# Kernel tuning notes

Measured on AMD Instinct MI355X. Metric: run time of the kernel, lower is better.

## Reference

```python
import jax, jax.numpy as jnp
import numpy as np

N_NODES = 8192
N_EDGES = 262144
HIDDEN = 256
EDGE_DIM = 64


def _lin(x, w, b=None):
    y = x @ w.T
    return y if b is None else y + b


def _gru(m, h, wih, whh, bih, bhh):
    # torch.nn.GRUCell math
    gi = m @ wih.T + bih
    gh = h @ whh.T + bhh
    i_r, i_z, i_n = jnp.split(gi, 3, axis=-1)
    h_r, h_z, h_n = jnp.split(gh, 3, axis=-1)
    r = jax.nn.sigmoid(i_r + h_r)
    z = jax.nn.sigmoid(i_z + h_z)
    n = jnp.tanh(i_n + r * h_n)
    return (1.0 - z) * n + z * h


def _dmpnn(x, src, dst, edge_attr, w_msg, wih, whh, bih, bhh):
    # message: W_msg([x_j ; e]) gathered at src, scatter-add to dst, GRU update
    msg = jnp.concatenate([x[src], edge_attr], axis=-1) @ w_msg.T  # [E,H]
    m = jax.ops.segment_sum(msg, dst, num_segments=x.shape[0])     # [N,H]
    return _gru(m, x, wih, whh, bih, bhh)


def _gin(x, src, dst, w1, b1, w2, b2):
    # GINConv with eps=0: mlp(x + sum_j x_j)
    agg = jax.ops.segment_sum(x[src], dst, num_segments=x.shape[0])
    return _lin(jax.nn.relu(_lin(x + agg, w1, b1)), w2, b2)


def setup_inputs():
    key = jax.random.key(0)
    ks = iter(jax.random.split(key, 48))
    def nrm(shape, scale=0.05):
        return jax.random.normal(next(ks), shape, dtype=jnp.float32) * scale
    H, ED = HIDDEN, EDGE_DIM
    inp = {}
    inp['x'] = nrm((N_NODES, H), 1.0)
    inp['edge_index'] = jax.random.randint(next(ks), (2, N_EDGES), 0, N_NODES, dtype=jnp.int32)
    inp['edge_attr'] = nrm((N_EDGES, ED), 1.0)
    inp['rc_mask'] = jax.random.randint(next(ks), (N_NODES,), 0, 20) == 0
    for i in (1, 2):
        inp[f'W_msg{i}'] = nrm((H, H + ED))
        inp[f'gru{i}_wih'] = nrm((3 * H, H))
        inp[f'gru{i}_whh'] = nrm((3 * H, H))
        inp[f'gru{i}_bih'] = jnp.zeros((3 * H,), jnp.float32)
        inp[f'gru{i}_bhh'] = jnp.zeros((3 * H,), jnp.float32)
    inp['gin_w1'] = nrm((3, H, H)); inp['gin_b1'] = jnp.zeros((3, H), jnp.float32)
    inp['gin_w2'] = nrm((3, H, H)); inp['gin_b2'] = jnp.zeros((3, H), jnp.float32)
    inp['proj_w'] = nrm((H, 3 * H)); inp['proj_b'] = jnp.zeros((H,), jnp.float32)
    for nm in ('q', 'k', 'v', 'o'):
        inp[f'{nm}_w'] = nrm((H, H)); inp[f'{nm}_b'] = jnp.zeros((H,), jnp.float32)
    inp['gate_w1'] = nrm((H // 2, H)); inp['gate_b1'] = jnp.zeros((H // 2,), jnp.float32)
    inp['gate_w2'] = nrm((1, H // 2)); inp['gate_b2'] = jnp.zeros((1,), jnp.float32)
    inp['skip_W'] = nrm((H, H))
    inp['sgru_wih'] = nrm((3 * H, H)); inp['sgru_whh'] = nrm((3 * H, H))
    inp['sgru_bih'] = jnp.zeros((3 * H,), jnp.float32); inp['sgru_bhh'] = jnp.zeros((3 * H,), jnp.float32)
    inp['rc_init'] = nrm((1, H)); inp['s_init'] = nrm((1, H))
    return inp


def reference(x, edge_index, edge_attr, rc_mask,
              W_msg1, gru1_wih, gru1_whh, gru1_bih, gru1_bhh,
              W_msg2, gru2_wih, gru2_whh, gru2_bih, gru2_bhh,
              gin_w1, gin_b1, gin_w2, gin_b2, proj_w, proj_b,
              q_w, q_b, k_w, k_b, v_w, v_b, o_w, o_b,
              gate_w1, gate_b1, gate_w2, gate_b2, skip_W,
              sgru_wih, sgru_whh, sgru_bih, sgru_bhh, rc_init, s_init):
    src, dst = edge_index[0], edge_index[1]
    N = x.shape[0]
    H = x.shape[1]
    # AtomDMPNN: two DMPNN layers
    h = _dmpnn(x, src, dst, edge_attr, W_msg1, gru1_wih, gru1_whh, gru1_bih, gru1_bhh)
    h = _dmpnn(h, src, dst, edge_attr, W_msg2, gru2_wih, gru2_whh, gru2_bih, gru2_bhh)
    # MixHop: 1-,2-,3-hop GINs, concat, project
    outs = []
    for i, hop in enumerate((1, 2, 3)):
        t = h
        for _ in range(hop):
            t = _gin(t, src, dst, gin_w1[i], gin_b1[i], gin_w2[i], gin_b2[i])
        outs.append(t)
    h_mix = _lin(jnp.concatenate(outs, axis=-1), proj_w, proj_b)  # [N,H]
    # add RC supernode (idx N) and S supernode (idx N+1)
    hh = jnp.concatenate([h_mix, rc_init, s_init], axis=0)  # [N+2,H]
    # GatedSkipBlock: masked non-RC atoms -> S
    atoms = hh[:N]
    alpha = jax.nn.sigmoid(_lin(jax.nn.relu(_lin(atoms, gate_w1, gate_b1)), gate_w2, gate_b2))  # [N,1]
    msgs = alpha * (atoms @ skip_W.T)
    non_rc = (~rc_mask).astype(hh.dtype)[:, None]
    m_sum = jnp.sum(msgs * non_rc, axis=0, keepdims=True)
    m_rc = hh[N:N + 1] @ skip_W.T  # h[-2:-1] is the RC node
    h_S = _gru(m_sum + m_rc, hh[N + 1:N + 2], sgru_wih, sgru_whh, sgru_bih, sgru_bhh)
    hh = hh.at[N + 1].set(h_S[0])
    # dense self-attention over all N+2 nodes
    q = _lin(hh, q_w, q_b)
    k = _lin(hh, k_w, k_b)
    v = _lin(hh, v_w, v_b)
    attn = jax.nn.softmax((q @ k.T) / jnp.sqrt(jnp.asarray(H, hh.dtype)), axis=-1)
    h_attn = hh + _lin(attn @ v, o_w, o_b)
    # jumping-knowledge max with zero-padded mixhop features
    h_pad = jnp.pad(h_mix, ((0, 2), (0, 0)))
    h_jk = jnp.maximum(h_pad, h_attn)
    return h_jk[N + 1]
```

## Files before the change

### kernel.cpp

```cpp
#include <hip/hip_runtime.h>
#include <hip/hip_bf16.h>

#define NN   8192
#define NE   262144
#define HD   256
#define NHH  8194

using f32x4  = __attribute__((ext_vector_type(4))) float;
using bf16x8 = __attribute__((ext_vector_type(8))) short;
typedef unsigned short u16;

#define GAS(p) ((const __attribute__((address_space(1))) void*)(p))
#define LAS(p) ((__attribute__((address_space(3))) void*)(p))

__device__ __forceinline__ u16 f2bf(float f) {
    unsigned u = __builtin_bit_cast(unsigned, f);
    u = (u + 0x7FFFu + ((u >> 16) & 1u)) >> 16;
    return (u16)u;
}
__device__ __forceinline__ float bf2f(u16 h) {
    return __builtin_bit_cast(float, (unsigned)h << 16);
}
__device__ __forceinline__ void split1(float a, u16& h, u16& l) {
    h = f2bf(a);
    l = f2bf(a - bf2f(h));
}
__device__ __forceinline__ void store_split4(u16* hi, u16* lo, size_t off, float4 v) {
    ushort4 h, l;
    split1(v.x, h.x, l.x); split1(v.y, h.y, l.y);
    split1(v.z, h.z, l.z); split1(v.w, h.w, l.w);
    *(ushort4*)(hi + off) = h;
    *(ushort4*)(lo + off) = l;
}
__device__ __forceinline__ void add4(float4& a, float4 b) {
    a.x += b.x; a.y += b.y; a.z += b.z; a.w += b.w;
}

__global__ void hist_kernel(const int* __restrict__ dst, int* __restrict__ cnt, int E) {
    int e = blockIdx.x * blockDim.x + threadIdx.x;
    if (e < E) atomicAdd(&cnt[dst[e]], 1);
}

__global__ __launch_bounds__(1024) void scan_kernel(const int* __restrict__ cnt, int* __restrict__ row_ptr) {
    __shared__ int sdata[1024];
    int tid = threadIdx.x;
    int v[8], local[8];
    int s = 0;
#pragma unroll
    for (int i = 0; i < 8; i++) v[i] = cnt[tid * 8 + i];
#pragma unroll
    for (int i = 0; i < 8; i++) { local[i] = s; s += v[i]; }
    sdata[tid] = s;
    __syncthreads();
    for (int off = 1; off < 1024; off <<= 1) {
        int t = (tid >= off) ? sdata[tid - off] : 0;
        __syncthreads();
        sdata[tid] += t;
        __syncthreads();
    }
    int base = (tid == 0) ? 0 : sdata[tid - 1];
#pragma unroll
    for (int i = 0; i < 8; i++) row_ptr[tid * 8 + i] = base + local[i];
    if (tid == 1023) row_ptr[8192] = sdata[1023];
}

__global__ void copy_int_kernel(const int* __restrict__ a, int* __restrict__ b, int n) {
    int i = blockIdx.x * blockDim.x + threadIdx.x;
    if (i < n) b[i] = a[i];
}

__global__ void fill_kernel(const int* __restrict__ dst, const int* __restrict__ src,
                            int* __restrict__ cursor, int* __restrict__ eids,
                            int* __restrict__ gsrc, int E) {
    int e = blockIdx.x * blockDim.x + threadIdx.x;
    if (e < E) {
        int pos = atomicAdd(&cursor[dst[e]], 1);
        eids[pos] = e;
        gsrc[pos] = src[e];
    }
}

struct SplitArgs {
    const float* src[11];
    u16* hi[11];
    u16* lo[11];
    int  off[12];
};
__global__ __launch_bounds__(256) void multisplit_kernel(SplitArgs a) {
    int blk = blockIdx.x;
    int s = 0;
#pragma unroll
    for (int t = 0; t < 11; ++t) if (blk >= a.off[t + 1]) s = t + 1;
    size_t i = ((size_t)(blk - a.off[s]) * 256 + threadIdx.x) * 4;
    float4 v = *(const float4*)(a.src[s] + i);
    store_split4(a.hi[s], a.lo[s], i, v);
}

__global__ void wtrans_split_kernel(const float* __restrict__ W, u16* __restrict__ outh,
                                    u16* __restrict__ outl, int R, int Cc) {
    int j = blockIdx.x * 256 + threadIdx.x;
    if (j >= R * Cc) return;
    int r = j % R, c = j / R;
    u16 h, l;
    split1(W[(size_t)r * Cc + c], h, l);
    outh[j] = h; outl[j] = l;
}

struct SegDuo {
    const float* T0; u16* oh0; u16* ol0; int self0;
    const float* T1; u16* oh1; u16* ol1; int self1; int nb0;
};
__global__ __launch_bounds__(256) void segsum128_wave_kernel(const int* __restrict__ row_ptr,
                                                             const int* __restrict__ idx,
                                                             SegDuo a) {
    int blk  = blockIdx.x;
    int seg  = blk / a.nb0;
    int lblk = blk - seg * a.nb0;
    const float* T; u16* oh; u16* ol; int self;
    if (seg >> 1) { T = a.T1; oh = a.oh1; ol = a.ol1; self = a.self1; }
    else          { T = a.T0; oh = a.oh0; ol = a.ol0; self = a.self0; }
    const int half = seg & 1;
    const int n    = lblk * 4 + (threadIdx.x >> 6);
    const int lane = threadIdx.x & 63;
    const int slot = lane >> 5;
    const size_t fo = (size_t)half * 128 + (size_t)(lane & 31) * 4;
    const int b = row_ptr[n], e = row_ptr[n + 1];
    float4 z4 = make_float4(0.f, 0.f, 0.f, 0.f);
    float4 a0 = z4, a1 = z4, a2 = z4, a3 = z4;
    int i = b + slot;
    for (; i + 6 < e; i += 8) {
        int s0 = idx[i], s1 = idx[i + 2], s2 = idx[i + 4], s3 = idx[i + 6];
        add4(a0, *(const float4*)(T + (size_t)s0 * HD + fo));
        add4(a1, *(const float4*)(T + (size_t)s1 * HD + fo));
        add4(a2, *(const float4*)(T + (size_t)s2 * HD + fo));
        add4(a3, *(const float4*)(T + (size_t)s3 * HD + fo));
    }
    for (; i < e; i += 2) {
        int s0 = idx[i];
        add4(a0, *(const float4*)(T + (size_t)s0 * HD + fo));
    }
    if (self && slot == 0) add4(a1, *(const float4*)(T + (size_t)n * HD + fo));
    add4(a0, a1); add4(a2, a3); add4(a0, a2);
    a0.x += __shfl_xor(a0.x, 32); a0.y += __shfl_xor(a0.y, 32);
    a0.z += __shfl_xor(a0.z, 32); a0.w += __shfl_xor(a0.w, 32);
    if (slot == 0) store_split4(oh, ol, (size_t)n * HD + fo, a0);
}

__global__ __launch_bounds__(256) void segsum64_wave_kernel(const int* __restrict__ row_ptr,
                                                            const int* __restrict__ idx,
                                                            const float* __restrict__ T,
                                                            u16* __restrict__ outh,
                                                            u16* __restrict__ outl) {
    const int n    = blockIdx.x * 4 + (threadIdx.x >> 6);
    const int lane = threadIdx.x & 63;
    const int g    = lane >> 4;
    const size_t fo = (size_t)(lane & 15) * 4;
    const int b = row_ptr[n], e = row_ptr[n + 1];
    float4 a0 = make_float4(0.f, 0.f, 0.f, 0.f);
    float4 a1 = a0;
    int i = b + g;
    for (; i + 4 < e; i += 8) {
        int s0 = idx[i], s1 = idx[i + 4];
        add4(a0, *(const float4*)(T + (size_t)s0 * 64 + fo));
        add4(a1, *(const float4*)(T + (size_t)s1 * 64 + fo));
    }
    if (i < e) {
        int s0 = idx[i];
        add4(a0, *(const float4*)(T + (size_t)s0 * 64 + fo));
    }
    add4(a0, a1);
    a0.x += __shfl_xor(a0.x, 16); a0.y += __shfl_xor(a0.y, 16);
    a0.z += __shfl_xor(a0.z, 16); a0.w += __shfl_xor(a0.w, 16);
    a0.x += __shfl_xor(a0.x, 32); a0.y += __shfl_xor(a0.y, 32);
    a0.z += __shfl_xor(a0.z, 32); a0.w += __shfl_xor(a0.w, 32);
    if (g == 0) store_split4(outh, outl, (size_t)n * 64 + fo, a0);
}

struct GDesc {
    const u16 *Ah, *Al, *Abh, *Abl, *Wh, *Wl;
    const float* bias;
    float* C; u16 *Chi, *Clo;
    int lda, ldab, Ka, Kb, ldw, ldc, M, flags, nbx, nblk;
};
struct GBatch { GDesc d[3]; int start[4]; };

#define LDSA0 0
#define LDSA1 8192
#define LDSW0 16384
#define LDSW1 20480
__global__ __launch_bounds__(256) void hgemm_kernel(GBatch b) {
    __shared__ __align__(16) u16 lds[24576];
    int s = (blockIdx.x >= (unsigned)b.start[1]) + (blockIdx.x >= (unsigned)b.start[2]);
    GDesc d = b.d[0];
    if (s == 1) d = b.d[1];
    else if (s == 2) d = b.d[2];

    int nwg = b.start[s + 1] - b.start[s];
    int o   = blockIdx.x - b.start[s];
    int q = nwg >> 3, r = nwg & 7;
    int xcd = o & 7;
    int base = (xcd < r) ? xcd * (q + 1) : r * (q + 1) + (xcd - r) * q;
    int wg = base + (o >> 3);
    int bx = wg % d.nbx, by = wg / d.nbx;

    const int tid  = threadIdx.x;
    const int wid  = tid >> 6;
    const int lane = tid & 63;
    const int lrow = lane & 15;
    const int ksel = lane >> 4;
    const int rswz = (lrow & 7) << 3;

    const int arow_l = wid * 8 + (lane >> 3);
    const int csrc8  = ((lane & 7) ^ ((lane >> 3) & 7)) * 8;

    const int nt = (d.Ka + d.Kb) >> 6;

    auto stage = [&](int t) {
        int kb = t << 6;
        const u16 *ph, *pl; int ld_; int kk;
        if (kb < d.Ka) { ph = d.Ah;  pl = d.Al;  ld_ = d.lda;  kk = kb; }
        else           { ph = d.Abh; pl = d.Abl; ld_ = d.ldab; kk = kb - d.Ka; }
#pragma unroll
        for (int i = 0; i < 4; ++i) {
            int row = i * 32 + arow_l;
            int rg  = min(by * 128 + row, d.M - 1);
            const u16* gah = ph + (size_t)rg * ld_ + kk + csrc8;
            const u16* gal = pl + (size_t)rg * ld_ + kk + csrc8;
            char* ba = (char*)lds + i * 4096 + wid * 1024;
            __builtin_amdgcn_global_load_lds(GAS(gah), LAS(ba), 16, 0, 0);
            __builtin_amdgcn_global_load_lds(GAS(gal), LAS(ba + LDSA1 * 2), 16, 0, 0);
        }
#pragma unroll
        for (int i = 0; i < 2; ++i) {
            int row = i * 32 + arow_l;
            size_t wo = (size_t)(bx * 64 + row) * d.ldw + kb + csrc8;
            const u16* gwh = d.Wh + wo;
            const u16* gwl = d.Wl + wo;
            char* bw = (char*)lds + LDSW0 * 2 + i * 4096 + wid * 1024;
            __builtin_amdgcn_global_load_lds(GAS(gwh), LAS(bw), 16, 0, 0);
            __builtin_amdgcn_global_load_lds(GAS(gwl), LAS(bw + (LDSW1 - LDSW0) * 2), 16, 0, 0);
        }
    };

    f32x4 acc[4][2] = {};
    const int fr0 = (wid >> 1) * 64;
    const int cr0 = (wid & 1) * 32;

    for (int t = 0; t < nt; ++t) {
        stage(t);
        __syncthreads();
#pragma unroll
        for (int ks = 0; ks < 2; ++ks) {
            bf16x8 fah[4], fal[4], fwh[2], fwl[2];
            const int ko = (ks * 32 + ksel * 8) ^ rswz;
#pragma unroll
            for (int fi = 0; fi < 4; ++fi) {
                int oo = (fr0 + fi * 16 + lrow) * 64 + ko;
                fah[fi] = *(const bf16x8*)(lds + LDSA0 + oo);
                fal[fi] = *(const bf16x8*)(lds + LDSA1 + oo);
            }
#pragma unroll
            for (int ci = 0; ci < 2; ++ci) {
                int oo = (cr0 + ci * 16 + lrow) * 64 + ko;
                fwh[ci] = *(const bf16x8*)(lds + LDSW0 + oo);
                fwl[ci] = *(const bf16x8*)(lds + LDSW1 + oo);
            }
#pragma unroll
            for (int fi = 0; fi < 4; ++fi)
#pragma unroll
                for (int ci = 0; ci < 2; ++ci) {
                    acc[fi][ci] = __builtin_amdgcn_mfma_f32_16x16x32_bf16(fah[fi], fwh[ci], acc[fi][ci], 0, 0, 0);
                    acc[fi][ci] = __builtin_amdgcn_mfma_f32_16x16x32_bf16(fah[fi], fwl[ci], acc[fi][ci], 0, 0, 0);
                    acc[fi][ci] = __builtin_amdgcn_mfma_f32_16x16x32_bf16(fal[fi], fwh[ci], acc[fi][ci], 0, 0, 0);
                }
        }
        __syncthreads();
    }

#pragma unroll
    for (int fi = 0; fi < 4; ++fi) {
        int rbase = by * 128 + fr0 + fi * 16 + (lane >> 4) * 4;
#pragma unroll
        for (int ci = 0; ci < 2; ++ci) {
            int col = bx * 64 + cr0 + ci * 16 + lrow;
#pragma unroll
            for (int j = 0; j < 4; ++j) {
                int rr = rbase + j;
                if (rr >= d.M) continue;
                float v = acc[fi][ci][j];
                size_t oo = (size_t)rr * d.ldc + col;
                if (d.flags & 2)    v += d.C[oo];
                else if (d.bias)    v += d.bias[col];
                if (d.flags & 1)    v = fmaxf(v, 0.f);
                if (d.C) d.C[oo] = v;
                if (d.Chi) { u16 hb, lb; split1(v, hb, lb); d.Chi[oo] = hb; d.Clo[oo] = lb; }
            }
        }
    }
}

__global__ void gru_combine_kernel(const float* __restrict__ gi, const float* __restrict__ gh,
                                   const float* __restrict__ hprev, float* __restrict__ hout,
                                   u16* __restrict__ hhi, u16* __restrict__ hlo, int total4) {
    int t = blockIdx.x * 256 + threadIdx.x;
    if (t >= total4) return;
    int i4  = t * 4;
    int row = i4 >> 8, f = i4 & 255;
    size_t b = (size_t)row * 768;
    float4 ir = *(const float4*)(gi + b + f);
    float4 iz = *(const float4*)(gi + b + 256 + f);
    float4 in_ = *(const float4*)(gi + b + 512 + f);
    float4 hr = *(const float4*)(gh + b + f);
    float4 hz = *(const float4*)(gh + b + 256 + f);
    float4 hn = *(const float4*)(gh + b + 512 + f);
    float4 hp = *(const float4*)(hprev + (size_t)row * HD + f);
    float4 hv;
#pragma unroll
    for (int j = 0; j < 4; ++j) {
        float irj = ((const float*)&ir)[j], izj = ((const float*)&iz)[j], inj = ((const float*)&in_)[j];
        float hrj = ((const float*)&hr)[j], hzj = ((const float*)&hz)[j], hnj = ((const float*)&hn)[j];
        float r = 1.f / (1.f + expf(-(irj + hrj)));
        float z = 1.f / (1.f + expf(-(izj + hzj)));
        float n = tanhf(inj + r * hnj);
        ((float*)&hv)[j] = (1.f - z) * n + z * ((const float*)&hp)[j];
    }
    size_t o = (size_t)row * HD + f;
    *(float4*)(hout + o) = hv;
    if (hhi) store_split4(hhi, hlo, o, hv);
}

__global__ void hhtail_kernel(const float* __restrict__ rc, const float* __restrict__ si,
                              float* __restrict__ hh, u16* __restrict__ hhi, u16* __restrict__ hlo) {
    int f = threadIdx.x;
    size_t o1 = (size_t)NN * HD + f, o2 = (size_t)(NN + 1) * HD + f;
    float a = rc[f], b = si[f];
    hh[o1] = a; hh[o2] = b;
    u16 h, l;
    split1(a, h, l); hhi[o1] = h; hlo[o1] = l;
    split1(b, h, l); hhi[o2] = h; hlo[o2] = l;
}

__global__ __launch_bounds__(256) void alpha_kernel(const float* __restrict__ g1, const float* __restrict__ gw2,
                                                    const float* __restrict__ gb2, const int* __restrict__ rcmask,
                                                    float* __restrict__ coef, int N) {
    int node = blockIdx.x * 4 + (threadIdx.x >> 6);
    int lane = threadIdx.x & 63;
    if (node >= N) return;
    float part = g1[(size_t)node * 128 + lane] * gw2[lane]
               + g1[(size_t)node * 128 + 64 + lane] * gw2[64 + lane];
    for (int off = 32; off > 0; off >>= 1) part += __shfl_down(part, off);
    if (lane == 0) {
        float a = 1.f / (1.f + expf(-(part + gb2[0])));
        coef[node] = rcmask[node] ? 0.f : a;
    }
}

__global__ __launch_bounds__(256) void colsum_kernel(const float* __restrict__ X, const float* __restrict__ coef,
                                                     float* __restrict__ out, int rows_total, int rows_per_blk) {
    int f  = threadIdx.x;
    int r0 = blockIdx.x * rows_per_blk;
    int r1 = r0 + rows_per_blk; if (r1 > rows_total) r1 = rows_total;
    float a0 = 0.f, a1 = 0.f;
    int r = r0;
    for (; r + 1 < r1; r += 2) {
        a0 += coef[r]     * X[(size_t)r * HD + f];
        a1 += coef[r + 1] * X[(size_t)(r + 1) * HD + f];
    }
    if (r < r1) a0 += coef[r] * X[(size_t)r * HD + f];
    atomicAdd(&out[f], a0 + a1);
}

__global__ __launch_bounds__(256) void gemv256_kernel(const float* __restrict__ M,
                                                      const float* __restrict__ vA,
                                                      const float* __restrict__ vB,
                                                      const float* __restrict__ bias,
                                                      float* __restrict__ out, int R) {
    int row  = blockIdx.x * 4 + (threadIdx.x >> 6);
    int lane = threadIdx.x & 63;
    if (row >= R) return;
    float4 v = *(const float4*)(vA + lane * 4);
    if (vB) {
        float4 b = *(const float4*)(vB + lane * 4);
        v.x += b.x; v.y += b.y; v.z += b.z; v.w += b.w;
    }
    float4 m = *(const float4*)(M + (size_t)row * 256 + lane * 4);
    float p = m.x * v.x + m.y * v.y + m.z * v.z + m.w * v.w;
    for (int off = 32; off > 0; off >>= 1) p += __shfl_down(p, off);
    if (lane == 0) out[row] = p + (bias ? bias[row] : 0.f);
}

__global__ void sgru_combine_kernel(const float* __restrict__ gi3, const float* __restrict__ gh3,
                                    const float* __restrict__ sinit,
                                    float* __restrict__ hh, u16* __restrict__ hhi, u16* __restrict__ hlo) {
    int f = threadIdx.x;
    float gir = gi3[f], giz = gi3[256 + f], gin_ = gi3[512 + f];
    float ghr = gh3[f], ghz = gh3[256 + f], ghn  = gh3[512 + f];
    float r = 1.f / (1.f + expf(-(gir + ghr)));
    float z = 1.f / (1.f + expf(-(giz + ghz)));
    float n = tanhf(gin_ + r * ghn);
    float hv = (1.f - z) * n + z * sinit[f];
    size_t o = (size_t)(NN + 1) * HD + f;
    hh[o] = hv;
    u16 h, l; split1(hv, h, l); hhi[o] = h; hlo[o] = l;
}

__global__ __launch_bounds__(256) void logits_kernel(const float* __restrict__ kall, const float* __restrict__ qrow,
                                                     float* __restrict__ logits, int n) {
    int j    = blockIdx.x * 4 + (threadIdx.x >> 6);
    int lane = threadIdx.x & 63;
    if (j >= n) return;
    float4 q = *(const float4*)(qrow + lane * 4);
    float4 k = *(const float4*)(kall + (size_t)j * HD + lane * 4);
    float part = q.x * k.x + q.y * k.y + q.z * k.z + q.w * k.w;
    for (int off = 32; off > 0; off >>= 1) part += __shfl_down(part, off);
    if (lane == 0) logits[j] = part * 0.0625f;
}

__global__ __launch_bounds__(1024) void softmax_prep_kernel(const float* __restrict__ logits, float* __restrict__ p,
                                                            float* __restrict__ scal, int n) {
    __shared__ float sd[1024];
    int tid = threadIdx.x;
    float mx = -1e30f;
    for (int j = tid; j < n; j += 1024) mx = fmaxf(mx, logits[j]);
    sd[tid] = mx;
    __syncthreads();
    for (int off = 512; off > 0; off >>= 1) { if (tid < off) sd[tid] = fmaxf(sd[tid], sd[tid + off]); __syncthreads(); }
    float m = sd[0];
    __syncthreads();
    float s = 0.f;
    for (int j = tid; j < n; j += 1024) { float e = expf(logits[j] - m); p[j] = e; s += e; }
    sd[tid] = s;
    __syncthreads();
    for (int off = 512; off > 0; off >>= 1) { if (tid < off) sd[tid] += sd[tid + off]; __syncthreads(); }
    if (tid == 0) scal[0] = sd[0];
}

__global__ __launch_bounds__(256) void final_gemv_kernel(const float* __restrict__ hh,
                                                         const float* __restrict__ ow,
                                                         const float* __restrict__ ob,
                                                         const float* __restrict__ ctx,
                                                         const float* __restrict__ scal,
                                                         float* __restrict__ out) {
    int row  = blockIdx.x * 4 + (threadIdx.x >> 6);
    int lane = threadIdx.x & 63;
    float4 c = *(const float4*)(ctx + lane * 4);
    float4 m = *(const float4*)(ow + (size_t)row * 256 + lane * 4);
    float p = m.x * c.x + m.y * c.y + m.z * c.z + m.w * c.w;
    for (int off = 32; off > 0; off >>= 1) p += __shfl_down(p, off);
    if (lane == 0) {
        float val = hh[(size_t)(NN + 1) * HD + row] + p / scal[0] + ob[row];
        out[row] = fmaxf(val, 0.f);
    }
}

extern "C" void kernel_launch(void* const* d_in, const int* in_sizes, int n_in,
                              void* d_out, int out_size, void* d_ws, size_t ws_size,
                              hipStream_t stream) {
    const float* x      = (const float*)d_in[0];
    const int*   ei     = (const int*)  d_in[1];
    const float* eattr  = (const float*)d_in[2];
    const int*   rcmask = (const int*)  d_in[3];
    const float* Wmsg1  = (const float*)d_in[4];
    const float* wih1   = (const float*)d_in[5];
    const float* whh1   = (const float*)d_in[6];
    const float* bih1   = (const float*)d_in[7];
    const float* bhh1   = (const float*)d_in[8];
    const float* Wmsg2  = (const float*)d_in[9];
    const float* wih2   = (const float*)d_in[10];
    const float* whh2   = (const float*)d_in[11];
    const float* bih2   = (const float*)d_in[12];
    const float* bhh2   = (const float*)d_in[13];
    const float* ginw1  = (const float*)d_in[14];
    const float* ginb1  = (const float*)d_in[15];
    const float* ginw2  = (const float*)d_in[16];
    const float* ginb2  = (const float*)d_in[17];
    const float* projw  = (const float*)d_in[18];
    const float* projb  = (const float*)d_in[19];
    const float* qw     = (const float*)d_in[20];
    const float* qb     = (const float*)d_in[21];
    const float* kw     = (const float*)d_in[22];
    const float* kb     = (const float*)d_in[23];
    const float* vw     = (const float*)d_in[24];
    const float* vb     = (const float*)d_in[25];
    const float* ow     = (const float*)d_in[26];
    const float* ob     = (const float*)d_in[27];
    const float* gatew1 = (const float*)d_in[28];
    const float* gateb1 = (const float*)d_in[29];
    const float* gatew2 = (const float*)d_in[30];
    const float* gateb2 = (const float*)d_in[31];
    const float* skipW  = (const float*)d_in[32];
    const float* swih   = (const float*)d_in[33];
    const float* swhh   = (const float*)d_in[34];
    const float* sbih   = (const float*)d_in[35];
    const float* sbhh   = (const float*)d_in[36];
    const float* rcinit = (const float*)d_in[37];
    const float* sinit  = (const float*)d_in[38];

    const int* src = ei;
    const int* dst = ei + NE;

    char*  w   = (char*)d_ws;
    size_t off = 0;
    auto alloc = [&](size_t bytes) -> void* {
        void* p = w + off;
        off = (off + bytes + 255) & ~(size_t)255;
        return p;
    };
    int*   cnt     = (int*)alloc((size_t)NN * 4);
    int*   row_ptr = (int*)alloc((size_t)(NN + 1) * 4);
    int*   eids    = (int*)alloc((size_t)NE * 4);
    int*   gsrc    = (int*)alloc((size_t)NE * 4);
    u16*   aeh     = (u16*)alloc((size_t)NN * 64 * 2);
    u16*   ael     = (u16*)alloc((size_t)NN * 64 * 2);
    u16*   shh_    = (u16*)alloc((size_t)NHH * HD * 2);
    u16*   shl_    = (u16*)alloc((size_t)NHH * HD * 2);
    u16*   gsh     = (u16*)alloc((size_t)NN * HD * 2);
    u16*   gsl     = (u16*)alloc((size_t)NN * HD * 2);
    u16*   gs2h    = (u16*)alloc((size_t)NN * HD * 2);
    u16*   gs2l    = (u16*)alloc((size_t)NN * HD * 2);
    u16*   msh     = (u16*)alloc((size_t)NN * HD * 2);
    u16*   msl     = (u16*)alloc((size_t)NN * HD * 2);
    u16*   ms2h    = (u16*)alloc((size_t)NN * HD * 2);
    u16*   ms2l    = (u16*)alloc((size_t)NN * HD * 2);
    float* h1      = (float*)alloc((size_t)NN * HD * 4);
    float* h2      = (float*)alloc((size_t)NN * HD * 4);
    float* gi      = (float*)alloc((size_t)NN * 768 * 4);
    float* gh      = (float*)alloc((size_t)NN * 768 * 4);
    float* hh      = (float*)alloc((size_t)NHH * HD * 4);
    float* coef    = (float*)alloc((size_t)NN * 4);
    float* wsum    = (float*)alloc(256 * 4);
    float* qrow    = (float*)alloc(256 * 4);
    float* logits  = (float*)alloc((size_t)NHH * 4);
    float* pbuf    = (float*)alloc((size_t)NHH * 4);
    float* scal    = (float*)alloc(256);
    float* ctx     = (float*)alloc(256 * 4);
    float* mvec    = (float*)alloc(256 * 4);
    float* gi3     = (float*)alloc(768 * 4);
    float* gh3     = (float*)alloc(768 * 4);

    auto walloc = [&](size_t nel, u16** h, u16** l) {
        *h = (u16*)alloc(nel * 2); *l = (u16*)alloc(nel * 2);
    };
    u16 *wm1Th, *wm1Tl, *wm2Th, *wm2Tl;
    u16 *wc1h, *wc1l, *wc2h, *wc2l;
    u16 *wi1h, *wi1l, *wh1h, *wh1l, *wi2h, *wi2l, *wh2h, *wh2l;
    u16 *g1h, *g1l, *g2h, *g2l, *pjh, *pjl, *gwh, *gwl, *kwh, *kwl, *vwh, *vwl;
    walloc(81920, &wm1Th, &wm1Tl); walloc(81920, &wm2Th, &wm2Tl);
    walloc(245760, &wc1h, &wc1l);  walloc(245760, &wc2h, &wc2l);
    walloc(196608, &wi1h, &wi1l);  walloc(196608, &wh1h, &wh1l);
    walloc(196608, &wi2h, &wi2l);  walloc(196608, &wh2h, &wh2l);
    walloc(196608, &g1h, &g1l);    walloc(196608, &g2h, &g2l);
    walloc(196608, &pjh, &pjl);    walloc(32768, &gwh, &gwl);
    walloc(65536, &kwh, &kwl);     walloc(65536, &vwh, &vwl);
    u16 *xh = shh_, *xl = shl_;

    u16*   u768h = (u16*)gh;
    u16*   u768l = u768h + (size_t)NN * 768;
    float* k_all = gh;
    float* v_all = gh + (size_t)NHH * HD;
    float* g1    = gh + (size_t)2 * NHH * HD;

    auto mkd = [&](const u16* Ah, const u16* Al, int lda,
                   const u16* Abh, const u16* Abl, int ldab, int Ka, int Kb,
                   const u16* Wh, const u16* Wl, int ldw, const float* bias,
                   float* C, u16* Chi, u16* Clo, int ldc,
                   int M, int Nc, int flags) -> GDesc {
        GDesc d;
        d.Ah = Ah; d.Al = Al; d.Abh = Abh; d.Abl = Abl; d.Wh = Wh; d.Wl = Wl;
        d.bias = bias; d.C = C; d.Chi = Chi; d.Clo = Clo;
        d.lda = lda; d.ldab = ldab; d.Ka = Ka; d.Kb = Kb; d.ldw = ldw; d.ldc = ldc;
        d.M = M; d.flags = flags; d.nbx = Nc / 64;
        d.nblk = d.nbx * ((M + 127) / 128);
        return d;
    };
    auto hg1 = [&](GDesc d0) {
        GBatch b; b.d[0] = d0; b.d[1] = d0; b.d[2] = d0;
        b.start[0] = 0; b.start[1] = d0.nblk; b.start[2] = d0.nblk; b.start[3] = d0.nblk;
        hgemm_kernel<<<b.start[3], 256, 0, stream>>>(b);
    };
    auto hg2 = [&](GDesc d0, GDesc d1) {
        GBatch b; b.d[0] = d0; b.d[1] = d1; b.d[2] = d1;
        b.start[0] = 0; b.start[1] = d0.nblk; b.start[2] = d0.nblk + d1.nblk; b.start[3] = b.start[2];
        hgemm_kernel<<<b.start[3], 256, 0, stream>>>(b);
    };
    auto hg3 = [&](GDesc d0, GDesc d1, GDesc d2) {
        GBatch b; b.d[0] = d0; b.d[1] = d1; b.d[2] = d2;
        b.start[0] = 0; b.start[1] = d0.nblk; b.start[2] = d0.nblk + d1.nblk;
        b.start[3] = b.start[2] + d2.nblk;
        hgemm_kernel<<<b.start[3], 256, 0, stream>>>(b);
    };
    auto seg1 = [&](const float* T, u16* oh, u16* ol, int self) {
        SegDuo a; a.T0 = T; a.oh0 = oh; a.ol0 = ol; a.self0 = self;
        a.T1 = T; a.oh1 = oh; a.ol1 = ol; a.self1 = self; a.nb0 = NN / 4;
        segsum128_wave_kernel<<<2 * (NN / 4), 256, 0, stream>>>(row_ptr, gsrc, a);
    };
    auto seg2 = [&](const float* T0, u16* oh0, u16* ol0, int s0,
                    const float* T1, u16* oh1, u16* ol1, int s1) {
        SegDuo a; a.T0 = T0; a.oh0 = oh0; a.ol0 = ol0; a.self0 = s0;
        a.T1 = T1; a.oh1 = oh1; a.ol1 = ol1; a.self1 = s1; a.nb0 = NN / 4;
        segsum128_wave_kernel<<<4 * (NN / 4), 256, 0, stream>>>(row_ptr, gsrc, a);
    };

    hipMemsetAsync(cnt, 0, (size_t)NN * 4, stream);
    hist_kernel<<<NE / 256, 256, 0, stream>>>(dst, cnt, NE);
    scan_kernel<<<1, 1024, 0, stream>>>(cnt, row_ptr);
    copy_int_kernel<<<NN / 256, 256, 0, stream>>>(row_ptr, cnt, NN);
    fill_kernel<<<NE / 256, 256, 0, stream>>>(dst, src, cnt, eids, gsrc, NE);
    segsum64_wave_kernel<<<NN / 4, 256, 0, stream>>>(row_ptr, eids, eattr, aeh, ael);

    {
        SplitArgs a;
        const float* srcs[11] = { x, wih1, whh1, wih2, whh2,
                                  ginw1, ginw2, projw, gatew1, kw, vw };
        u16* his[11] = { xh, wi1h, wh1h, wi2h, wh2h, g1h, g2h, pjh, gwh, kwh, vwh };
        u16* los[11] = { xl, wi1l, wh1l, wi2l, wh2l, g1l, g2l, pjl, gwl, kwl, vwl };
        const int blocks[11] = { 2048, 192, 192, 192, 192, 192, 192, 192, 32, 64, 64 };
        int acc = 0;
        for (int t = 0; t < 11; ++t) { a.src[t] = srcs[t]; a.hi[t] = his[t]; a.lo[t] = los[t]; a.off[t] = acc; acc += blocks[t]; }
        a.off[11] = acc;
        multisplit_kernel<<<acc, 256, 0, stream>>>(a);
    }
    wtrans_split_kernel<<<(81920 + 255) / 256, 256, 0, stream>>>(Wmsg1, wm1Th, wm1Tl, 256, 320);
    wtrans_split_kernel<<<(81920 + 255) / 256, 256, 0, stream>>>(Wmsg2, wm2Th, wm2Tl, 256, 320);
    hg2(mkd(wi1h, wi1l, HD, nullptr, nullptr, 0, HD, 0, wm1Th, wm1Tl, HD, nullptr,
            nullptr, wc1h, wc1l, 320, 768, 320, 0),
        mkd(wi2h, wi2l, HD, nullptr, nullptr, 0, HD, 0, wm2Th, wm2Tl, HD, nullptr,
            nullptr, wc2h, wc2l, 320, 768, 320, 0));

    seg1(x, gsh, gsl, 0);
    hg2(mkd(gsh, gsl, HD, aeh, ael, 64, HD, 64, wc1h, wc1l, 320, bih1,
            gi, nullptr, nullptr, 768, NN, 768, 0),
        mkd(shh_, shl_, HD, nullptr, nullptr, 0, HD, 0, wh1h, wh1l, HD, bhh1,
            gh, nullptr, nullptr, 768, NN, 768, 0));
    gru_combine_kernel<<<NN * HD / 1024, 256, 0, stream>>>(gi, gh, x, h1, gs2h, gs2l, NN * HD / 4);

    seg1(h1, gsh, gsl, 0);
    hg2(mkd(gsh, gsl, HD, aeh, ael, 64, HD, 64, wc2h, wc2l, 320, bih2,
            gi, nullptr, nullptr, 768, NN, 768, 0),
        mkd(gs2h, gs2l, HD, nullptr, nullptr, 0, HD, 0, wh2h, wh2l, HD, bhh2,
            gh, nullptr, nullptr, 768, NN, 768, 0));
    gru_combine_kernel<<<NN * HD / 1024, 256, 0, stream>>>(gi, gh, h1, h2, nullptr, nullptr, NN * HD / 4);

    seg1(h2, gsh, gsl, 1);
    hg1(mkd(gsh, gsl, HD, nullptr, nullptr, 0, HD, 0, g1h, g1l, HD, ginb1,
            nullptr, u768h, u768l, 768, NN, 768, 1));
    hg3(mkd(u768h, u768l, 768, nullptr, nullptr, 0, HD, 0, g2h, g2l, HD, ginb2,
            nullptr, msh, msl, HD, NN, HD, 0),
        mkd(u768h + 256, u768l + 256, 768, nullptr, nullptr, 0, HD, 0, g2h + 65536, g2l + 65536, HD, ginb2 + 256,
            h1, nullptr, nullptr, HD, NN, HD, 0),
        mkd(u768h + 512, u768l + 512, 768, nullptr, nullptr, 0, HD, 0, g2h + 131072, g2l + 131072, HD, ginb2 + 512,
            h2, nullptr, nullptr, HD, NN, HD, 0));
    hg1(mkd(msh, msl, HD, nullptr, nullptr, 0, HD, 0, pjh, pjl, 768, projb,
            hh, nullptr, nullptr, HD, NN, HD, 0));
    seg2(h1, gsh, gsl, 1, h2, gs2h, gs2l, 1);
    hg2(mkd(gsh, gsl, HD, nullptr, nullptr, 0, HD, 0, g1h + 65536, g1l + 65536, HD, ginb1 + 256,
            nullptr, msh, msl, HD, NN, HD, 1),
        mkd(gs2h, gs2l, HD, nullptr, nullptr, 0, HD, 0, g1h + 131072, g1l + 131072, HD, ginb1 + 512,
            nullptr, ms2h, ms2l, HD, NN, HD, 1));
    hg2(mkd(msh, msl, HD, nullptr, nullptr, 0, HD, 0, g2h + 65536, g2l + 65536, HD, ginb2 + 256,
            nullptr, gsh, gsl, HD, NN, HD, 0),
        mkd(ms2h, ms2l, HD, nullptr, nullptr, 0, HD, 0, g2h + 131072, g2l + 131072, HD, ginb2 + 512,
            h1, nullptr, nullptr, HD, NN, HD, 0));
    hg1(mkd(gsh, gsl, HD, nullptr, nullptr, 0, HD, 0, pjh + 256, pjl + 256, 768, nullptr,
            hh, nullptr, nullptr, HD, NN, HD, 2));
    seg1(h1, gs2h, gs2l, 1);
    hg1(mkd(gs2h, gs2l, HD, nullptr, nullptr, 0, HD, 0, g1h + 131072, g1l + 131072, HD, ginb1 + 512,
            nullptr, ms2h, ms2l, HD, NN, HD, 1));
    hg1(mkd(ms2h, ms2l, HD, nullptr, nullptr, 0, HD, 0, g2h + 131072, g2l + 131072, HD, ginb2 + 512,
            nullptr, gs2h, gs2l, HD, NN, HD, 0));
    hg1(mkd(gs2h, gs2l, HD, nullptr, nullptr, 0, HD, 0, pjh + 512, pjl + 512, 768, nullptr,
            hh, shh_, shl_, HD, NN, HD, 2));
    hhtail_kernel<<<1, 256, 0, stream>>>(rcinit, sinit, hh, shh_, shl_);

    hg1(mkd(shh_, shl_, HD, nullptr, nullptr, 0, HD, 0, gwh, gwl, HD, gateb1,
            g1, nullptr, nullptr, 128, NN, 128, 1));
    alpha_kernel<<<NN / 4, 256, 0, stream>>>(g1, gatew2, gateb2, rcmask, coef, NN);
    hipMemsetAsync(wsum, 0, 256 * 4, stream);
    colsum_kernel<<<256, 256, 0, stream>>>(hh, coef, wsum, NN, 32);
    gemv256_kernel<<<64, 256, 0, stream>>>(skipW, wsum, rcinit, nullptr, mvec, 256);
    gemv256_kernel<<<192, 256, 0, stream>>>(swih, mvec, nullptr, sbih, gi3, 768);
    gemv256_kernel<<<192, 256, 0, stream>>>(swhh, sinit, nullptr, sbhh, gh3, 768);
    sgru_combine_kernel<<<1, 256, 0, stream>>>(gi3, gh3, sinit, hh, shh_, shl_);

    hg2(mkd(shh_, shl_, HD, nullptr, nullptr, 0, HD, 0, kwh, kwl, HD, kb,
            k_all, nullptr, nullptr, HD, NHH, HD, 0),
        mkd(shh_, shl_, HD, nullptr, nullptr, 0, HD, 0, vwh, vwl, HD, vb,
            v_all, nullptr, nullptr, HD, NHH, HD, 0));
    gemv256_kernel<<<64, 256, 0, stream>>>(qw, hh + (size_t)(NN + 1) * HD, nullptr, qb, qrow, 256);
    logits_kernel<<<(NHH + 3) / 4, 256, 0, stream>>>(k_all, qrow, logits, NHH);
    softmax_prep_kernel<<<1, 1024, 0, stream>>>(logits, pbuf, scal, NHH);
    hipMemsetAsync(ctx, 0, 256 * 4, stream);
    colsum_kernel<<<(NHH + 31) / 32, 256, 0, stream>>>(v_all, pbuf, ctx, NHH, 32);
    final_gemv_kernel<<<64, 256, 0, stream>>>(hh, ow, ob, ctx, scal, (float*)d_out);
}
```

Baseline: 546.4 us.

## Batch independent MixHop GEMMs into grouped launches and deepen segsum unroll

Reorders the MixHop GIN/projection GEMM sequence so independent GEMMs (projection accumulations and GIN first layers) share grouped hg2/hg3 launches, using scratch buffers carved from the gh workspace to avoid overwriting live inputs. This cuts the number of small GEMM launches and gives each launch more blocks to fill the GPU. The 128-wide segment-sum kernel also unrolls to 8 independent gathers per iteration to keep more memory loads in flight. The cost is more register use, and the scratch aliasing within gh has to be correct: gh must not still hold live data at that point.

```diff
diff --git a/kernel.cpp b/kernel.cpp
--- a/kernel.cpp
+++ b/kernel.cpp
@@ -127,20 +127,27 @@
     const int b = row_ptr[n], e = row_ptr[n + 1];
     float4 z4 = make_float4(0.f, 0.f, 0.f, 0.f);
     float4 a0 = z4, a1 = z4, a2 = z4, a3 = z4;
+    float4 a4 = z4, a5 = z4, a6 = z4, a7 = z4;
     int i = b + slot;
-    for (; i + 6 < e; i += 8) {
-        int s0 = idx[i], s1 = idx[i + 2], s2 = idx[i + 4], s3 = idx[i + 6];
+    for (; i + 14 < e; i += 16) {
+        int s0 = idx[i],      s1 = idx[i + 2],  s2 = idx[i + 4],  s3 = idx[i + 6];
+        int s4 = idx[i + 8],  s5 = idx[i + 10], s6 = idx[i + 12], s7 = idx[i + 14];
         add4(a0, *(const float4*)(T + (size_t)s0 * HD + fo));
         add4(a1, *(const float4*)(T + (size_t)s1 * HD + fo));
         add4(a2, *(const float4*)(T + (size_t)s2 * HD + fo));
         add4(a3, *(const float4*)(T + (size_t)s3 * HD + fo));
+        add4(a4, *(const float4*)(T + (size_t)s4 * HD + fo));
+        add4(a5, *(const float4*)(T + (size_t)s5 * HD + fo));
+        add4(a6, *(const float4*)(T + (size_t)s6 * HD + fo));
+        add4(a7, *(const float4*)(T + (size_t)s7 * HD + fo));
     }
     for (; i < e; i += 2) {
         int s0 = idx[i];
         add4(a0, *(const float4*)(T + (size_t)s0 * HD + fo));
     }
     if (self && slot == 0) add4(a1, *(const float4*)(T + (size_t)n * HD + fo));
-    add4(a0, a1); add4(a2, a3); add4(a0, a2);
+    add4(a0, a1); add4(a2, a3); add4(a4, a5); add4(a6, a7);
+    add4(a0, a2); add4(a4, a6); add4(a0, a4);
     a0.x += __shfl_xor(a0.x, 32); a0.y += __shfl_xor(a0.y, 32);
     a0.z += __shfl_xor(a0.z, 32); a0.w += __shfl_xor(a0.w, 32);
     if (slot == 0) store_split4(oh, ol, (size_t)n * HD + fo, a0);
@@ -556,6 +563,10 @@
 
     u16*   u768h = (u16*)gh;
     u16*   u768l = u768h + (size_t)NN * 768;
+    u16*   sAh   = (u16*)gh;
+    u16*   sAl   = sAh + (size_t)NN * HD;
+    u16*   sBh   = sAh + (size_t)2 * NN * HD;
+    u16*   sBl   = sAh + (size_t)3 * NN * HD;
     float* k_all = gh;
     float* v_all = gh + (size_t)NHH * HD;
     float* g1    = gh + (size_t)2 * NHH * HD;
@@ -650,21 +661,21 @@
             h1, nullptr, nullptr, HD, NN, HD, 0),
         mkd(u768h + 512, u768l + 512, 768, nullptr, nullptr, 0, HD, 0, g2h + 131072, g2l + 131072, HD, ginb2 + 512,
             h2, nullptr, nullptr, HD, NN, HD, 0));
-    hg1(mkd(msh, msl, HD, nullptr, nullptr, 0, HD, 0, pjh, pjl, 768, projb,
-            hh, nullptr, nullptr, HD, NN, HD, 0));
     seg2(h1, gsh, gsl, 1, h2, gs2h, gs2l, 1);
-    hg2(mkd(gsh, gsl, HD, nullptr, nullptr, 0, HD, 0, g1h + 65536, g1l + 65536, HD, ginb1 + 256,
-            nullptr, msh, msl, HD, NN, HD, 1),
+    hg3(mkd(msh, msl, HD, nullptr, nullptr, 0, HD, 0, pjh, pjl, 768, projb,
+            hh, nullptr, nullptr, HD, NN, HD, 0),
+        mkd(gsh, gsl, HD, nullptr, nullptr, 0, HD, 0, g1h + 65536, g1l + 65536, HD, ginb1 + 256,
+            nullptr, sAh, sAl, HD, NN, HD, 1),
         mkd(gs2h, gs2l, HD, nullptr, nullptr, 0, HD, 0, g1h + 131072, g1l + 131072, HD, ginb1 + 512,
-            nullptr, ms2h, ms2l, HD, NN, HD, 1));
-    hg2(mkd(msh, msl, HD, nullptr, nullptr, 0, HD, 0, g2h + 65536, g2l + 65536, HD, ginb2 + 256,
+            nullptr, sBh, sBl, HD, NN, HD, 1));
+    hg2(mkd(sAh, sAl, HD, nullptr, nullptr, 0, HD, 0, g2h + 65536, g2l + 65536, HD, ginb2 + 256,
             nullptr, gsh, gsl, HD, NN, HD, 0),
-        mkd(ms2h, ms2l, HD, nullptr, nullptr, 0, HD, 0, g2h + 131072, g2l + 131072, HD, ginb2 + 512,
+        mkd(sBh, sBl, HD, nullptr, nullptr, 0, HD, 0, g2h + 131072, g2l + 131072, HD, ginb2 + 512,
             h1, nullptr, nullptr, HD, NN, HD, 0));
-    hg1(mkd(gsh, gsl, HD, nullptr, nullptr, 0, HD, 0, pjh + 256, pjl + 256, 768, nullptr,
-            hh, nullptr, nullptr, HD, NN, HD, 2));
     seg1(h1, gs2h, gs2l, 1);
-    hg1(mkd(gs2h, gs2l, HD, nullptr, nullptr, 0, HD, 0, g1h + 131072, g1l + 131072, HD, ginb1 + 512,
+    hg2(mkd(gsh, gsl, HD, nullptr, nullptr, 0, HD, 0, pjh + 256, pjl + 256, 768, nullptr,
+            hh, nullptr, nullptr, HD, NN, HD, 2),
+        mkd(gs2h, gs2l, HD, nullptr, nullptr, 0, HD, 0, g1h + 131072, g1l + 131072, HD, ginb1 + 512,
             nullptr, ms2h, ms2l, HD, NN, HD, 1));
     hg1(mkd(ms2h, ms2l, HD, nullptr, nullptr, 0, HD, 0, g2h + 131072, g2l + 131072, HD, ginb2 + 512,
             nullptr, gs2h, gs2l, HD, NN, HD, 0));
```

After: 554.6 us. No clear change (+1.5%).
